# Optimization experiments

Hardware: AMD Instinct MI355X
Metric: run time of the kernel (lower is better)

Reference implementation:

```python
import jax, jax.numpy as jnp
import numpy as np

VOCAB, EMB_DIM, KERNEL_NUM = 400000, 50, 21
SIGMA, EXACT_SIGMA = 0.1, 0.001
EPS = 1e-12  # matches torch F.normalize clamp_min eps


def _kernel_params():
    mus, sigmas = [], []
    for i in range(KERNEL_NUM):
        mu = 1.0 / (KERNEL_NUM - 1) + 2.0 * i / (KERNEL_NUM - 1) - 1.0
        s = SIGMA
        if mu > 1.0:
            s = EXACT_SIGMA
            mu = 1.0
        mus.append(mu)
        sigmas.append(s)
    return mus, sigmas

MUS, SIGMAS = _kernel_params()


def setup_inputs() -> dict:
    key = jax.random.key(0)
    ks = jax.random.split(key, 7)
    B, LQ, LD = 4096, 30, 128
    q1 = jax.random.randint(ks[0], (B, LQ), 0, VOCAB, dtype=jnp.int32)
    d1 = jax.random.randint(ks[1], (B, LD), 0, VOCAB, dtype=jnp.int32)
    q2 = jax.random.randint(ks[2], (B, LQ), 0, VOCAB, dtype=jnp.int32)
    d2 = jax.random.randint(ks[3], (B, LD), 0, VOCAB, dtype=jnp.int32)
    emb = jax.random.normal(ks[4], (VOCAB, EMB_DIM), dtype=jnp.float32)
    mlp_w = jax.random.normal(ks[5], (1, KERNEL_NUM), dtype=jnp.float32) / np.sqrt(KERNEL_NUM)
    mlp_b = jax.random.normal(ks[6], (1,), dtype=jnp.float32) * 0.01
    return {"q1": q1, "d1": d1, "q2": q2, "d2": d2,
            "emb": emb, "mlp_w": mlp_w, "mlp_b": mlp_b}


def _l2norm(x):
    # torch F.normalize(p=2, dim=-1): x / max(||x||, eps)
    n = jnp.sqrt(jnp.sum(x * x, axis=-1, keepdims=True))
    return x / jnp.maximum(n, EPS)


def _predict(q, d, emb, mlp_w, mlp_b):
    eq = _l2norm(emb[q])              # [B, Lq, D]
    ed = _l2norm(emb[d])              # [B, Ld, D]
    mm = jnp.einsum('bld,brd->blr', eq, ed)  # cosine match matrix [B, Lq, Ld]
    # 21 Gaussian RBF kernels, soft-TF pooling: sum over doc, log1p, sum over query
    km = [jnp.sum(jnp.log1p(jnp.sum(
            jnp.exp(-(mm - mu) ** 2 / (2.0 * s * s)), axis=-1)), axis=-1)
          for mu, s in zip(MUS, SIGMAS)]
    kernels_out = jnp.stack(km, axis=1)      # [B, 21]
    return kernels_out @ mlp_w.T + mlp_b      # [B, 1]


def reference(q1, d1, q2, d2, emb, mlp_w, mlp_b):
    logits_1 = _predict(q1, d1, emb, mlp_w, mlp_b)
    logits_2 = _predict(q2, d2, emb, mlp_w, mlp_b)
    return jax.nn.sigmoid(logits_1 - logits_2)  # [B, 1]
```

## Files before the change

### kernel.cpp

```cpp
#include <hip/hip_runtime.h>
#include <hip/hip_fp16.h>

#define BATCH 4096
#define LQ 30
#define LD 128
#define EMB 50
#define ROWS 160
#define KN 21
#define THREADS 512
#define K10 14.426950408889634f
#define C50 72.134752044448169f
#define KW  144.26950408889634f

typedef __attribute__((ext_vector_type(8))) _Float16 half8;
typedef __attribute__((ext_vector_type(4))) float f32x4;

#define EXP2(x) __builtin_amdgcn_exp2f(x)
#define SHW(row, c) (((row) << 5) + ((((c) ^ ((row) & 7))) << 2))

__device__ __constant__ float Gv[20] = {
  1.928749847963918e-22f, 2.576757109154981e-18f, 1.266416554909418e-14f,
  2.269996488124243e-11f, 1.522997974471263e-08f, 3.726653172078671e-06f,
  3.354626279025119e-04f, 1.110899653824231e-02f, 1.353352832366127e-01f,
  6.065306597126334e-01f, 1.0f,
  6.065306597126334e-01f, 1.353352832366127e-01f, 1.110899653824231e-02f,
  3.354626279025119e-04f, 3.726653172078671e-06f, 1.522997974471263e-08f,
  2.269996488124243e-11f, 1.266416554909418e-14f, 2.576757109154981e-18f
};

__device__ __forceinline__ unsigned pack2(float a, float b) {
  __half2 h = __floats2half2_rn(a, b);
  return *reinterpret_cast<unsigned*>(&h);
}

__global__ void knrm_pair_kernel(
    const int* __restrict__ q1, const int* __restrict__ d1,
    const int* __restrict__ q2, const int* __restrict__ d2,
    const float* __restrict__ emb, const float* __restrict__ mlp_w,
    const float* __restrict__ mlp_b, float* __restrict__ logits)
{
  __shared__ unsigned int shw[ROWS * 32];
  __shared__ alignas(16) int toks[ROWS];
  __shared__ float kacc2[2][4][16][KN];

  const int b = blockIdx.x;
  const int pair = blockIdx.y;
  const int tid = threadIdx.x;
  const int* __restrict__ qp = pair ? q2 : q1;
  const int* __restrict__ dp = pair ? d2 : d1;

  if (tid < 2 * ROWS) {
    const int row = tid >> 1;
    const int p = tid & 1;
    int tok = -1;
    if (row < LQ) tok = qp[b * LQ + row];
    else if (row >= 32) tok = dp[b * LD + (row - 32)];
    if (p == 0) toks[row] = tok;

    float4 e[6];
    float2 tail = make_float2(0.f, 0.f);
    float ss = 0.f;
    if (tok >= 0) {
      const float* bp = emb + (long)tok * EMB + p * 24;
      #pragma unroll
      for (int c = 0; c < 6; ++c) e[c] = *(const float4*)(bp + 4 * c);
      if (p) tail = *(const float2*)(emb + (long)tok * EMB + 48);
      #pragma unroll
      for (int c = 0; c < 6; ++c)
        ss += e[c].x*e[c].x + e[c].y*e[c].y + e[c].z*e[c].z + e[c].w*e[c].w;
      ss += tail.x*tail.x + tail.y*tail.y;
    } else {
      #pragma unroll
      for (int c = 0; c < 6; ++c) e[c] = make_float4(0.f, 0.f, 0.f, 0.f);
    }
    ss += __shfl_xor(ss, 1);
    const float scale = 1.0f / fmaxf(sqrtf(ss), 1e-12f);
    #pragma unroll
    for (int cc = 0; cc < 3; ++cc) {
      const float4 a = e[2 * cc], b4 = e[2 * cc + 1];
      uint4 w4;
      w4.x = pack2(a.x * scale, a.y * scale);
      w4.y = pack2(a.z * scale, a.w * scale);
      w4.z = pack2(b4.x * scale, b4.y * scale);
      w4.w = pack2(b4.z * scale, b4.w * scale);
      *(uint4*)&shw[SHW(row, p * 3 + cc)] = w4;
    }
    if (p) {
      uint4 t6 = {pack2(tail.x * scale, tail.y * scale), 0u, 0u, 0u};
      *(uint4*)&shw[SHW(row, 6)] = t6;
      uint4 z = {0u, 0u, 0u, 0u};
      *(uint4*)&shw[SHW(row, 7)] = z;
    }
  }
  __syncthreads();

  const int lane = tid & 63;
  const int w = tid >> 6;
  const int qtile = w >> 2;
  const int dpair = w & 3;
  const int col = lane & 15;
  const int kgrp = lane >> 4;

  const int qrow = qtile * 16 + col;
  const half8 Bq0 = *(const half8*)&shw[SHW(qrow, kgrp)];
  const half8 Bq1 = *(const half8*)&shw[SHW(qrow, 4 + kgrp)];
  const int qtok = toks[qrow];

  const int arow0 = 32 + dpair * 16 + col;
  const int arow1 = arow0 + 64;
  const half8 A00 = *(const half8*)&shw[SHW(arow0, kgrp)];
  const half8 A01 = *(const half8*)&shw[SHW(arow0, 4 + kgrp)];
  const half8 A10 = *(const half8*)&shw[SHW(arow1, kgrp)];
  const half8 A11 = *(const half8*)&shw[SHW(arow1, 4 + kgrp)];

  f32x4 acc0 = {0.0f, 0.0f, 0.0f, 0.0f};
  f32x4 acc1 = {0.0f, 0.0f, 0.0f, 0.0f};
  acc0 = __builtin_amdgcn_mfma_f32_16x16x32_f16(A00, Bq0, acc0, 0, 0, 0);
  acc0 = __builtin_amdgcn_mfma_f32_16x16x32_f16(A01, Bq1, acc0, 0, 0, 0);
  acc1 = __builtin_amdgcn_mfma_f32_16x16x32_f16(A10, Bq0, acc1, 0, 0, 0);
  acc1 = __builtin_amdgcn_mfma_f32_16x16x32_f16(A11, Bq1, acc1, 0, 0, 0);

  const int dbase0 = 32 + dpair * 16 + kgrp * 4;
  const int4 dt0 = *(const int4*)&toks[dbase0];
  const int4 dt1 = *(const int4*)&toks[dbase0 + 64];
  float cnt = 0.0f;
  cnt += (dt0.x == qtok) ? 1.0f : 0.0f;
  cnt += (dt0.y == qtok) ? 1.0f : 0.0f;
  cnt += (dt0.z == qtok) ? 1.0f : 0.0f;
  cnt += (dt0.w == qtok) ? 1.0f : 0.0f;
  cnt += (dt1.x == qtok) ? 1.0f : 0.0f;
  cnt += (dt1.y == qtok) ? 1.0f : 0.0f;
  cnt += (dt1.z == qtok) ? 1.0f : 0.0f;
  cnt += (dt1.w == qtok) ? 1.0f : 0.0f;

  float macc[20];
  #pragma unroll
  for (int k = 0; k < 20; ++k) macc[k] = 0.0f;

  const float xs[8] = {acc0[0], acc0[1], acc0[2], acc0[3],
                       acc1[0], acc1[1], acc1[2], acc1[3]};
  #pragma unroll
  for (int r = 0; r < 8; ++r) {
    const float x = xs[r];
    const float t  = x - 0.05f;
    const float tt = t * t;
    const float varg = -C50 * tt;
    const float v = EXP2(varg);
    const float T = EXP2(K10 * t);
    const float wd = EXP2(fmaf(-KW, t, varg));
    const float T2 = T * T, T3 = T2 * T, T4 = T2 * T2;
    macc[10] += v;
    macc[11] = fmaf(v, T,  macc[11]);
    macc[12] = fmaf(v, T2, macc[12]);
    macc[13] = fmaf(v, T3, macc[13]);
    float pu = v * T4;
    macc[14] += pu;
    macc[15] = fmaf(pu, T,  macc[15]);
    macc[16] = fmaf(pu, T2, macc[16]);
    macc[17] = fmaf(pu, T3, macc[17]);
    pu *= T4;
    macc[18] += pu;
    macc[19] = fmaf(pu, T,  macc[19]);
    macc[0] += wd;
    macc[1] = fmaf(wd, T,  macc[1]);
    macc[2] = fmaf(wd, T2, macc[2]);
    macc[3] = fmaf(wd, T3, macc[3]);
    float qd = wd * T4;
    macc[4] += qd;
    macc[5] = fmaf(qd, T,  macc[5]);
    macc[6] = fmaf(qd, T2, macc[6]);
    macc[7] = fmaf(qd, T3, macc[7]);
    qd *= T4;
    macc[8] += qd;
    macc[9] = fmaf(qd, T,  macc[9]);
  }

  #pragma unroll
  for (int k = 0; k < 20; ++k) {
    macc[k] += __shfl_xor(macc[k], 16);
    macc[k] += __shfl_xor(macc[k], 32);
  }
  cnt += __shfl_xor(cnt, 16);
  cnt += __shfl_xor(cnt, 32);

  if (lane < 16) {
    #pragma unroll
    for (int k = 0; k < 20; ++k)
      kacc2[qtile][dpair][lane][k] = macc[k] * Gv[k];
    kacc2[qtile][dpair][lane][20] = cnt;
  }
  __syncthreads();

  if (tid < 64) {
    float s = 0.0f;
    if (tid < 32) {
      const int qt = tid >> 4, q = tid & 15;
      if (qt * 16 + q < LQ) {
        #pragma unroll
        for (int k = 0; k < KN; ++k) {
          const float S = kacc2[qt][0][q][k] + kacc2[qt][1][q][k] +
                          kacc2[qt][2][q][k] + kacc2[qt][3][q][k];
          s = fmaf(mlp_w[k], __logf(1.0f + S), s);
        }
      }
    }
    s += __shfl_xor(s, 1);
    s += __shfl_xor(s, 2);
    s += __shfl_xor(s, 4);
    s += __shfl_xor(s, 8);
    s += __shfl_xor(s, 16);
    s += __shfl_xor(s, 32);
    if (tid == 0) logits[pair * BATCH + b] = s + mlp_b[0];
  }
}

__global__ void knrm_combine_kernel(const float* __restrict__ logits,
                                    float* __restrict__ out) {
  int i = blockIdx.x * 256 + threadIdx.x;
  if (i < BATCH) {
    float z = logits[i] - logits[BATCH + i];
    out[i] = 1.0f / (1.0f + __expf(-z));
  }
}

extern "C" void kernel_launch(void* const* d_in, const int* in_sizes, int n_in,
                              void* d_out, int out_size, void* d_ws, size_t ws_size,
                              hipStream_t stream) {
  const int* q1 = (const int*)d_in[0];
  const int* d1 = (const int*)d_in[1];
  const int* q2 = (const int*)d_in[2];
  const int* d2 = (const int*)d_in[3];
  const float* emb = (const float*)d_in[4];
  const float* mlp_w = (const float*)d_in[5];
  const float* mlp_b = (const float*)d_in[6];
  float* out = (float*)d_out;
  float* logits = (float*)d_ws;

  dim3 grid(BATCH, 2);
  knrm_pair_kernel<<<grid, THREADS, 0, stream>>>(q1, d1, q2, d2, emb, mlp_w, mlp_b, logits);
  knrm_combine_kernel<<<(BATCH + 255) / 256, 256, 0, stream>>>(logits, out);
}
```

Measured before the change: 82.23 us.

## Precompute normalized fp16 embedding table and gather rows directly into LDS

Adds a pre-pass kernel that L2-normalizes every embedding row and stores it as a padded 64-half row in workspace. The main kernel then gathers these 128-byte rows straight into shared memory instead of loading fp32 rows and normalizing per block. This aims to cut gather bytes and per-block normalization work. In exchange it converts the entire vocabulary on every call, adding a full-table read and write plus an extra launch. It only runs if the workspace is large enough.

```diff
diff --git a/kernel.cpp b/kernel.cpp
--- a/kernel.cpp
+++ b/kernel.cpp
@@ -1,6 +1,7 @@
 #include <hip/hip_runtime.h>
 #include <hip/hip_fp16.h>
 
+#define VOCAB 400000
 #define BATCH 4096
 #define LQ 30
 #define LD 128
@@ -33,11 +34,49 @@
   return *reinterpret_cast<unsigned*>(&h);
 }
 
+__global__ void knrm_convert_kernel(const float* __restrict__ emb,
+                                    __half* __restrict__ tab) {
+  const int tid = threadIdx.x;
+  const int row = blockIdx.x * 128 + (tid >> 1);
+  const int p = tid & 1;
+  const float* bp = emb + (long)row * EMB + p * 24;
+  float4 e[6];
+  float2 tail = make_float2(0.f, 0.f);
+  #pragma unroll
+  for (int c = 0; c < 6; ++c) e[c] = *(const float4*)(bp + 4 * c);
+  if (p) tail = *(const float2*)(emb + (long)row * EMB + 48);
+  float ss = 0.f;
+  #pragma unroll
+  for (int c = 0; c < 6; ++c)
+    ss += e[c].x*e[c].x + e[c].y*e[c].y + e[c].z*e[c].z + e[c].w*e[c].w;
+  ss += tail.x*tail.x + tail.y*tail.y;
+  ss += __shfl_xor(ss, 1);
+  const float scale = 1.0f / fmaxf(sqrtf(ss), 1e-12f);
+  __half* out = tab + ((long)row << 6);
+  #pragma unroll
+  for (int cc = 0; cc < 3; ++cc) {
+    const float4 a = e[2 * cc], b4 = e[2 * cc + 1];
+    uint4 w4;
+    w4.x = pack2(a.x * scale, a.y * scale);
+    w4.y = pack2(a.z * scale, a.w * scale);
+    w4.z = pack2(b4.x * scale, b4.y * scale);
+    w4.w = pack2(b4.z * scale, b4.w * scale);
+    *(uint4*)(out + ((p * 3 + cc) << 3)) = w4;
+  }
+  if (p) {
+    uint4 t6 = {pack2(tail.x * scale, tail.y * scale), 0u, 0u, 0u};
+    *(uint4*)(out + (6 << 3)) = t6;
+    uint4 z = {0u, 0u, 0u, 0u};
+    *(uint4*)(out + (7 << 3)) = z;
+  }
+}
+
 __global__ void knrm_pair_kernel(
     const int* __restrict__ q1, const int* __restrict__ d1,
     const int* __restrict__ q2, const int* __restrict__ d2,
     const float* __restrict__ emb, const float* __restrict__ mlp_w,
-    const float* __restrict__ mlp_b, float* __restrict__ logits)
+    const float* __restrict__ mlp_b, float* __restrict__ logits,
+    const __half* __restrict__ tab, const int fastpath)
 {
   __shared__ unsigned int shw[ROWS * 32];
   __shared__ alignas(16) int toks[ROWS];
@@ -49,29 +88,43 @@
   const int* __restrict__ qp = pair ? q2 : q1;
   const int* __restrict__ dp = pair ? d2 : d1;
 
-  if (tid < 2 * ROWS) {
+  if (tid < ROWS) {
+    int t = -1;
+    if (tid < LQ) t = qp[b * LQ + tid];
+    else if (tid >= 32) t = dp[b * LD + (tid - 32)];
+    toks[tid] = t;
+  }
+  __syncthreads();
+
+  if (fastpath) {
+    const int wv = tid >> 6, ln = tid & 63;
+    const int c = ln & 7, rl = ln >> 3;
+    for (int it = wv; it < 20; it += 8) {
+      const int r = it * 8 + rl;
+      int tok = toks[r];
+      tok = tok < 0 ? 0 : tok;
+      const uint4 val = *(const uint4*)(tab + ((long)tok << 6) + (c << 3));
+      *(uint4*)&shw[SHW(r, c)] = val;
+    }
+  } else if (tid < 2 * ROWS) {
     const int row = tid >> 1;
     const int p = tid & 1;
-    int tok = -1;
-    if (row < LQ) tok = qp[b * LQ + row];
-    else if (row >= 32) tok = dp[b * LD + (row - 32)];
-    if (p == 0) toks[row] = tok;
-
+    const int tok = toks[row];
     float4 e[6];
     float2 tail = make_float2(0.f, 0.f);
     float ss = 0.f;
     if (tok >= 0) {
       const float* bp = emb + (long)tok * EMB + p * 24;
       #pragma unroll
-      for (int c = 0; c < 6; ++c) e[c] = *(const float4*)(bp + 4 * c);
+      for (int cc = 0; cc < 6; ++cc) e[cc] = *(const float4*)(bp + 4 * cc);
       if (p) tail = *(const float2*)(emb + (long)tok * EMB + 48);
       #pragma unroll
-      for (int c = 0; c < 6; ++c)
-        ss += e[c].x*e[c].x + e[c].y*e[c].y + e[c].z*e[c].z + e[c].w*e[c].w;
+      for (int cc = 0; cc < 6; ++cc)
+        ss += e[cc].x*e[cc].x + e[cc].y*e[cc].y + e[cc].z*e[cc].z + e[cc].w*e[cc].w;
       ss += tail.x*tail.x + tail.y*tail.y;
     } else {
       #pragma unroll
-      for (int c = 0; c < 6; ++c) e[c] = make_float4(0.f, 0.f, 0.f, 0.f);
+      for (int cc = 0; cc < 6; ++cc) e[cc] = make_float4(0.f, 0.f, 0.f, 0.f);
     }
     ss += __shfl_xor(ss, 1);
     const float scale = 1.0f / fmaxf(sqrtf(ss), 1e-12f);
@@ -235,8 +288,16 @@
   const float* mlp_b = (const float*)d_in[6];
   float* out = (float*)d_out;
   float* logits = (float*)d_ws;
+  __half* tab = (__half*)((char*)d_ws + 32768);
+
+  const size_t need = 32768 + (size_t)VOCAB * 64 * sizeof(__half);
+  const int fast = (ws_size >= need) ? 1 : 0;
+
+  if (fast)
+    knrm_convert_kernel<<<VOCAB / 128, 256, 0, stream>>>(emb, tab);
 
   dim3 grid(BATCH, 2);
-  knrm_pair_kernel<<<grid, THREADS, 0, stream>>>(q1, d1, q2, d2, emb, mlp_w, mlp_b, logits);
+  knrm_pair_kernel<<<grid, THREADS, 0, stream>>>(q1, d1, q2, d2, emb, mlp_w,
+                                                 mlp_b, logits, tab, fast);
   knrm_combine_kernel<<<(BATCH + 255) / 256, 256, 0, stream>>>(logits, out);
 }
```

Result: slower. 90.30 us (+9.8%).
